# Optimization experiments

Hardware: AMD Instinct MI355X
Metric: run time of the kernel (lower is better)

The kernel has to match this reference:

```python
import jax, jax.numpy as jnp
import numpy as np

B = 16384
C = 512          # mean candidate count per sample
T = B * C        # total flat logits length (static)


def _seg_ce(logits, counts, gt, valid, B):
    """Segmented cross-entropy over variable-length candidate sets.
    logits: [T] flat concatenated logits; counts: [B] segment lengths (sum == T);
    gt: [B] target index within each segment; valid: [B] bool mask.
    Returns (mean loss over valid samples, n_correct, n_valid)."""
    Ttot = logits.shape[0]
    offsets = jnp.cumsum(counts) - counts                       # [B] start of each segment
    seg = jnp.repeat(jnp.arange(B), counts, total_repeat_length=Ttot)  # [T] segment ids
    segmax = jax.ops.segment_max(logits, seg, num_segments=B)   # [B]
    ex = jnp.exp(logits - segmax[seg])
    Z = jax.ops.segment_sum(ex, seg, num_segments=B)            # [B]
    lse = jnp.log(Z) + segmax                                   # [B] logsumexp per segment
    # target logit: clamp position for safety; invalid rows are masked out anyway
    pos = offsets + jnp.clip(gt, 0, jnp.maximum(counts - 1, 0))
    ce = lse - logits[pos]                                      # [B]
    in_range = (gt >= 0) & (gt < counts)
    vmask = (counts > 0) & in_range & valid
    n_valid = vmask.sum()
    loss = jnp.where(vmask, ce, 0.0).sum() / jnp.maximum(n_valid, 1)
    # argmax within each segment (first occurrence, matching torch.argmax)
    local = jnp.arange(Ttot) - offsets[seg]
    is_max = logits == segmax[seg]
    arg = jax.ops.segment_min(jnp.where(is_max, local, Ttot), seg, num_segments=B)
    n_correct = (vmask & (arg == gt)).sum()
    return loss, n_correct, n_valid


def setup_inputs() -> dict:
    key = jax.random.key(0)
    ks = jax.random.split(key, 8)
    # counts alternate C+32 / C-32 so sum == B*C exactly (static T)
    counts = jnp.where(jnp.arange(B) % 2 == 0, C + 32, C - 32).astype(jnp.int32)
    sys_logits = jax.random.normal(ks[0], (T,), dtype=jnp.float32)
    bar_logits = jax.random.normal(ks[1], (T,), dtype=jnp.float32)
    gt_system_idx = jax.random.randint(ks[2], (B,), 0, C - 32).astype(jnp.int32)
    gt_bar_in_sys = jax.random.randint(ks[3], (B,), 0, C - 32).astype(jnp.int32)
    note_positions = jax.random.uniform(ks[4], (B,), dtype=jnp.float32)
    gt_note_position = jax.random.uniform(ks[5], (B,), dtype=jnp.float32)
    gt_valid = jax.random.bernoulli(ks[6], 0.97, (B,))
    return {
        'sys_logits': sys_logits, 'sys_counts': counts,
        'bar_logits': bar_logits, 'bar_counts': counts,
        'note_positions': note_positions,
        'gt_system_idx': gt_system_idx, 'gt_bar_in_sys': gt_bar_in_sys,
        'gt_note_position': gt_note_position, 'gt_valid': gt_valid,
        'log_var_sys': jnp.zeros((), jnp.float32),
        'log_var_bar': jnp.zeros((), jnp.float32),
        'log_var_note': jnp.zeros((), jnp.float32),
    }


def reference(sys_logits, sys_counts, bar_logits, bar_counts, note_positions,
              gt_system_idx, gt_bar_in_sys, gt_note_position, gt_valid,
              log_var_sys, log_var_bar, log_var_note):
    Bn = gt_system_idx.shape[0]
    sys_loss, sys_correct, n_valid = _seg_ce(sys_logits, sys_counts, gt_system_idx, gt_valid, Bn)
    bar_loss, bar_correct, n_valid_bar = _seg_ce(bar_logits, bar_counts, gt_bar_in_sys, gt_valid, Bn)
    # note position MSE over valid samples (bar_valid == gt_valid here)
    m = gt_valid
    nsel = m.sum()
    sq = jnp.where(m, (note_positions - gt_note_position) ** 2, 0.0)
    note_loss = jnp.where(nsel > 0, sq.sum() / jnp.maximum(nsel, 1), 0.0)
    prec_sys = jnp.exp(-log_var_sys)
    prec_bar = jnp.exp(-log_var_bar)
    prec_note = jnp.exp(-log_var_note)
    loss = (0.5 * prec_sys * sys_loss + 0.5 * log_var_sys
            + 0.5 * prec_bar * bar_loss + 0.5 * log_var_bar
            + 0.5 * prec_note * note_loss + 0.5 * log_var_note)
    sys_acc = sys_correct / jnp.maximum(n_valid, 1)
    bar_acc = bar_correct / jnp.maximum(n_valid_bar, 1)
    return (loss, sys_loss, bar_loss, note_loss, sys_acc, bar_acc,
            prec_sys, prec_bar, prec_note)
```

## Files before the change

kernel.cpp:

```cpp
#include <hip/hip_runtime.h>
#include <math.h>

#define SCAN_BLOCKS 64
#define DESC_BASE 512
#define NOTE_SQ   256
#define NOTE_CNT  320

__device__ __forceinline__ bool is_valid(const void* gv, int flag, int i) {
  if (flag == 0) return ((const int*)gv)[i] != 0;
  if (flag == 1) return ((const unsigned char*)gv)[i] != 0;
  return ((const float*)gv)[i] != 0.0f;
}

__global__ __launch_bounds__(256)
void uwl_scan_desc(const int* __restrict__ c_sys, const int* __restrict__ c_bar,
                   const int* __restrict__ gt_sys, const int* __restrict__ gt_bar,
                   const void* __restrict__ gv,
                   const float* __restrict__ npos, const float* __restrict__ gnp,
                   int B, int* __restrict__ wsI, float* __restrict__ wsF) {
  const int blk = blockIdx.x;
  const int lane = threadIdx.x & 63;
  const int wid = threadIdx.x >> 6;
  __shared__ int s_flag;
  __shared__ int baseS, baseB;
  __shared__ int ws1[4], ws2[4];
  __shared__ float fsq[4];
  const int chunk = (B + SCAN_BLOCKS - 1) / SCAN_BLOCKS;
  const int start = blk * chunk;
  const int end = (start + chunk < B) ? start + chunk : B;
  int bs = 0, bb = 0;
  {
    const int s4 = start >> 2;
    const int4* cs4 = (const int4*)c_sys;
    const int4* cb4 = (const int4*)c_bar;
    for (int j = threadIdx.x; j < s4; j += 256) {
      const int4 a = cs4[j]; bs += a.x + a.y + a.z + a.w;
      const int4 b = cb4[j]; bb += b.x + b.y + b.z + b.w;
    }
    if (threadIdx.x < (start & 3)) {
      bs += c_sys[(s4 << 2) + threadIdx.x];
      bb += c_bar[(s4 << 2) + threadIdx.x];
    }
  }
#pragma unroll
  for (int d = 1; d < 64; d <<= 1) {
    bs += __shfl_xor(bs, d, 64);
    bb += __shfl_xor(bb, d, 64);
  }
  if (lane == 0) { ws1[wid] = bs; ws2[wid] = bb; }
  if (threadIdx.x < 64) {
    int nw = B / 4; if (nw > 64) nw = 64; if (nw < 1) nw = 1;
    const unsigned int x =
        (threadIdx.x < nw) ? ((const unsigned int*)gv)[threadIdx.x] : 0u;
    const bool all01 = __all(x <= 1u);
    const bool allf = __all(x == 0u || x == 0x3F800000u);
    if (threadIdx.x == 0) s_flag = all01 ? 0 : (allf ? 2 : 1);
  }
  if (blk == 0) {
    if (threadIdx.x >= 1 && threadIdx.x <= 8) wsI[threadIdx.x * 16] = 0;
    if (threadIdx.x == 9) wsI[144] = 0;
  }
  __syncthreads();
  if (threadIdx.x == 0) {
    baseS = ws1[0] + ws1[1] + ws1[2] + ws1[3];
    baseB = ws2[0] + ws2[1] + ws2[2] + ws2[3];
  }
  __syncthreads();
  const int flag = s_flag;
  int carry1 = baseS, carry2 = baseB;
  int4* descS = (int4*)(wsI + DESC_BASE);
  int4* descB = descS + B;
  for (int base = start; base < end; base += 256) {
    const int idx = base + threadIdx.x;
    const bool ok = idx < end;
    const int x1 = ok ? c_sys[idx] : 0;
    const int x2 = ok ? c_bar[idx] : 0;
    int o1 = x1, o2 = x2;
#pragma unroll
    for (int d = 1; d < 64; d <<= 1) {
      const int v1 = __shfl_up(o1, d, 64);
      const int v2 = __shfl_up(o2, d, 64);
      if (lane >= d) { o1 += v1; o2 += v2; }
    }
    if (lane == 63) { ws1[wid] = o1; ws2[wid] = o2; }
    __syncthreads();
    int w1 = 0, w2 = 0;
    for (int w = 0; w < wid; ++w) { w1 += ws1[w]; w2 += ws2[w]; }
    if (ok) {
      const int g1 = gt_sys[idx], g2 = gt_bar[idx];
      const bool v = is_valid(gv, flag, idx);
      descS[idx] = make_int4(carry1 + w1 + o1 - x1, x1, g1,
                             (x1 > 0 && g1 >= 0 && g1 < x1 && v) ? 1 : 0);
      descB[idx] = make_int4(carry2 + w2 + o2 - x2, x2, g2,
                             (x2 > 0 && g2 >= 0 && g2 < x2 && v) ? 1 : 0);
    }
    carry1 += ws1[0] + ws1[1] + ws1[2] + ws1[3];
    carry2 += ws2[0] + ws2[1] + ws2[2] + ws2[3];
    __syncthreads();
  }
  float sq = 0.f; int cnt = 0;
  for (int i = start + threadIdx.x; i < end; i += 256) {
    if (is_valid(gv, flag, i)) {
      const float d = npos[i] - gnp[i];
      sq += d * d; cnt += 1;
    }
  }
#pragma unroll
  for (int d = 1; d < 64; d <<= 1) {
    sq += __shfl_xor(sq, d, 64);
    cnt += __shfl_xor(cnt, d, 64);
  }
  if (lane == 0) { fsq[wid] = sq; ws1[wid] = cnt; }
  __syncthreads();
  if (threadIdx.x == 0) {
    wsF[NOTE_SQ + blk] = fsq[0] + fsq[1] + fsq[2] + fsq[3];
    wsI[NOTE_CNT + blk] = ws1[0] + ws1[1] + ws1[2] + ws1[3];
  }
}

__global__ __launch_bounds__(256)
void uwl_ce_kernel(const float* __restrict__ sys_lg, const float* __restrict__ bar_lg,
                   int B, int* __restrict__ wsI, float* __restrict__ wsF) {
  const int wave = __builtin_amdgcn_readfirstlane(
      (int)((blockIdx.x * blockDim.x + threadIdx.x) >> 6));
  const int lane = threadIdx.x & 63;
  if (wave >= 2 * B) return;
  const int4 d4 = ((const int4*)(wsI + DESC_BASE))[wave];
  const float* lg = (wave < B) ? sys_lg : bar_lg;
  const int off_i = d4.x, count = d4.y, gt = d4.z, vld = d4.w;
  const long long off = off_i;

  float m = -INFINITY;
  float s = 0.f;
  float tl = 0.f;
  const bool regpath = (count >= 4) && (count <= 576) &&
                       ((off_i & 3) == 0) && ((count & 3) == 0);
  if (regpath) {
    const float4* p = (const float4*)(lg + off);
    const int emax = (count >> 2) - 1;
    float vals[8];
#pragma unroll
    for (int k = 0; k < 2; ++k) {
      const int e4 = (k << 6) + lane;
      const int ec = (e4 > emax) ? emax : e4;
      const float4 v = p[ec];
      const bool live = (e4 <= emax);
      vals[4 * k]     = live ? v.x : -INFINITY;
      vals[4 * k + 1] = live ? v.y : -INFINITY;
      vals[4 * k + 2] = live ? v.z : -INFINITY;
      vals[4 * k + 3] = live ? v.w : -INFINITY;
    }
    const int ti = 512 + lane;
    const int tic = (ti < count) ? ti : (count - 1);
    const float tvr = lg[off + tic];
    const float tv = (ti < count) ? tvr : -INFINITY;
#pragma unroll
    for (int k = 0; k < 8; ++k) m = fmaxf(m, vals[k]);
    m = fmaxf(m, tv);
#pragma unroll
    for (int k = 0; k < 8; ++k) s += __expf(vals[k]);
    s += __expf(tv);
    const int gts = vld ? gt : 0;
    float pick;
    int srclane;
    if (gts < 512) {
      const int q = ((gts >> 8) << 2) | (gts & 3);
      pick = vals[0];
#pragma unroll
      for (int i = 1; i < 8; ++i) pick = (i == q) ? vals[i] : pick;
      srclane = (gts >> 2) & 63;
    } else {
      pick = tv;
      srclane = gts - 512;
    }
    tl = __shfl(pick, srclane, 64);
  } else {
    for (int i = lane; i < count; i += 64) {
      const float v = lg[off + i];
      m = fmaxf(m, v);
      s += __expf(v);
    }
    if (vld) {
      const float t0 = (lane == 0) ? lg[off + gt] : 0.f;
      tl = __shfl(t0, 0, 64);
    }
  }
#pragma unroll
  for (int d = 1; d < 64; d <<= 1) {
    s += __shfl_xor(s, d, 64);
    m = fmaxf(m, __shfl_xor(m, d, 64));
  }
  if (lane == 0) {
    float ce = 0.f, code = 0.f;
    if (vld) {
      ce = __logf(s) - tl;
      code = (tl == m) ? 3.f : 1.f;
    }
    ((float2*)(wsF + DESC_BASE + 8 * B))[wave] = make_float2(ce, code);
  }
}

__global__ __launch_bounds__(256)
void uwl_reduce_kernel(const float* __restrict__ lvs_p, const float* __restrict__ lvb_p,
                       const float* __restrict__ lvn_p,
                       int B, int* wsI, float* wsF, float* __restrict__ out) {
  const float4* pw4 = (const float4*)(wsF + DESC_BASE + 8 * B);
  float ces = 0.f, ceb = 0.f;
  int nvs = 0, cs = 0, nvb = 0, cb = 0;
  const int stride = gridDim.x * blockDim.x;
  for (int j = blockIdx.x * blockDim.x + threadIdx.x; j < B; j += stride) {
    const float4 v = pw4[j];
    const int e0 = 2 * j, e1 = 2 * j + 1;
    const int c0 = (int)v.y, c1 = (int)v.w;
    if (e0 < B) { ces += v.x; nvs += c0 & 1; cs += c0 >> 1; }
    else        { ceb += v.x; nvb += c0 & 1; cb += c0 >> 1; }
    if (e1 < B) { ces += v.z; nvs += c1 & 1; cs += c1 >> 1; }
    else        { ceb += v.z; nvb += c1 & 1; cb += c1 >> 1; }
  }
  float sq = 0.f; int cnt = 0;
  if (blockIdx.x == 0 && threadIdx.x < SCAN_BLOCKS) {
    sq = wsF[NOTE_SQ + threadIdx.x];
    cnt = wsI[NOTE_CNT + threadIdx.x];
  }
#pragma unroll
  for (int d = 1; d < 64; d <<= 1) {
    ces += __shfl_xor(ces, d, 64);
    ceb += __shfl_xor(ceb, d, 64);
    nvs += __shfl_xor(nvs, d, 64);
    cs  += __shfl_xor(cs,  d, 64);
    nvb += __shfl_xor(nvb, d, 64);
    cb  += __shfl_xor(cb,  d, 64);
    sq  += __shfl_xor(sq,  d, 64);
    cnt += __shfl_xor(cnt, d, 64);
  }
  if ((threadIdx.x & 63) == 0) {
    atomicAdd(&wsI[16], nvs);
    atomicAdd(&wsI[32], cs);
    atomicAdd(&wsF[48], ces);
    atomicAdd(&wsI[64], nvb);
    atomicAdd(&wsI[80], cb);
    atomicAdd(&wsF[96], ceb);
    atomicAdd(&wsI[112], cnt);
    atomicAdd(&wsF[128], sq);
  }
  __syncthreads();
  if (threadIdx.x == 0) {
    __threadfence();
    const int t = atomicAdd(&wsI[144], 1);
    if (t == (int)gridDim.x - 1) {
      __threadfence();
      const int fnvs = atomicAdd(&wsI[16], 0);
      const int fcs  = atomicAdd(&wsI[32], 0);
      const int fnvb = atomicAdd(&wsI[64], 0);
      const int fcb  = atomicAdd(&wsI[80], 0);
      const int fnn  = atomicAdd(&wsI[112], 0);
      const float fces = atomicAdd(&wsF[48], 0.f);
      const float fceb = atomicAdd(&wsF[96], 0.f);
      const float fsq  = atomicAdd(&wsF[128], 0.f);
      const float sys_loss = fces / (float)(fnvs > 1 ? fnvs : 1);
      const float bar_loss = fceb / (float)(fnvb > 1 ? fnvb : 1);
      const float note_loss = (fnn > 0) ? fsq / (float)fnn : 0.f;
      const float lvs = lvs_p[0], lvb = lvb_p[0], lvn = lvn_p[0];
      const float ps = expf(-lvs), pb = expf(-lvb), pn = expf(-lvn);
      out[0] = 0.5f * (ps * sys_loss + lvs + pb * bar_loss + lvb + pn * note_loss + lvn);
      out[1] = sys_loss;
      out[2] = bar_loss;
      out[3] = note_loss;
      out[4] = (float)fcs / (float)(fnvs > 1 ? fnvs : 1);
      out[5] = (float)fcb / (float)(fnvb > 1 ? fnvb : 1);
      out[6] = ps;
      out[7] = pb;
      out[8] = pn;
    }
  }
}

extern "C" void kernel_launch(void* const* d_in, const int* in_sizes, int n_in,
                              void* d_out, int out_size, void* d_ws, size_t ws_size,
                              hipStream_t stream) {
  const float* sys_lg = (const float*)d_in[0];
  const int*   c_sys  = (const int*)d_in[1];
  const float* bar_lg = (const float*)d_in[2];
  const int*   c_bar  = (const int*)d_in[3];
  const float* npos   = (const float*)d_in[4];
  const int*   gt_sys = (const int*)d_in[5];
  const int*   gt_bar = (const int*)d_in[6];
  const float* gnp    = (const float*)d_in[7];
  const void*  gv     = d_in[8];
  const float* lvs    = (const float*)d_in[9];
  const float* lvb    = (const float*)d_in[10];
  const float* lvn    = (const float*)d_in[11];
  const int B = in_sizes[1];

  int*   wsI = (int*)d_ws;
  float* wsF = (float*)d_ws;

  uwl_scan_desc<<<SCAN_BLOCKS, 256, 0, stream>>>(c_sys, c_bar, gt_sys, gt_bar, gv,
                                                 npos, gnp, B, wsI, wsF);

  const long long nthreads = (long long)(2 * B) * 64;
  const int nblocks = (int)((nthreads + 255) / 256);
  uwl_ce_kernel<<<nblocks, 256, 0, stream>>>(sys_lg, bar_lg, B, wsI, wsF);

  uwl_reduce_kernel<<<64, 256, 0, stream>>>(lvs, lvb, lvn, B, wsI, wsF, (float*)d_out);
}
```

Before: 130.0 us.

## Widen scan grid, split scan waves by role, make CE kernel grid-stride

The scan/descriptor kernel now runs on 256 blocks instead of 64. Within each block, wave 0 does the segment prefix scan with a single-wave carry and wave 1 computes the note MSE, removing the block-wide barriers inside the scan loop. The CE kernel becomes a persistent grid-stride loop over segments, capped at 2048 blocks, instead of launching one wave per segment. The workspace offsets move to make room for 256 per-block note partials. The trade-offs are two idle waves per scan block and more redundant prefix-count reads across the larger scan grid.

Result: no change. 131.6 us (+1.3%).

```diff
diff --git a/kernel.cpp b/kernel.cpp
--- a/kernel.cpp
+++ b/kernel.cpp
@@ -1,10 +1,10 @@
 #include <hip/hip_runtime.h>
 #include <math.h>
 
-#define SCAN_BLOCKS 64
-#define DESC_BASE 512
+#define SCAN_BLOCKS 256
 #define NOTE_SQ   256
-#define NOTE_CNT  320
+#define NOTE_CNT  512
+#define DESC_BASE 1024
 
 __device__ __forceinline__ bool is_valid(const void* gv, int flag, int i) {
   if (flag == 0) return ((const int*)gv)[i] != 0;
@@ -19,27 +19,38 @@
                    const float* __restrict__ npos, const float* __restrict__ gnp,
                    int B, int* __restrict__ wsI, float* __restrict__ wsF) {
   const int blk = blockIdx.x;
-  const int lane = threadIdx.x & 63;
-  const int wid = threadIdx.x >> 6;
+  const int tid = threadIdx.x;
+  const int lane = tid & 63;
+  const int wid = tid >> 6;
   __shared__ int s_flag;
-  __shared__ int baseS, baseB;
-  __shared__ int ws1[4], ws2[4];
-  __shared__ float fsq[4];
+  __shared__ int sS[4], sB[4];
   const int chunk = (B + SCAN_BLOCKS - 1) / SCAN_BLOCKS;
-  const int start = blk * chunk;
-  const int end = (start + chunk < B) ? start + chunk : B;
+  const int start0 = blk * chunk;
+  const int start = (start0 < B) ? start0 : B;
+  const int end = (start0 + chunk < B) ? start0 + chunk : B;
+  if (tid < 64) {
+    int nw = B / 4; if (nw > 64) nw = 64; if (nw < 1) nw = 1;
+    const unsigned int x = (tid < nw) ? ((const unsigned int*)gv)[tid] : 0u;
+    const bool all01 = __all(x <= 1u);
+    const bool allf = __all(x == 0u || x == 0x3F800000u);
+    if (tid == 0) s_flag = all01 ? 0 : (allf ? 2 : 1);
+  }
+  if (blk == 0) {
+    if (tid >= 1 && tid <= 8) wsI[tid * 16] = 0;
+    if (tid == 9) wsI[144] = 0;
+  }
   int bs = 0, bb = 0;
   {
     const int s4 = start >> 2;
     const int4* cs4 = (const int4*)c_sys;
     const int4* cb4 = (const int4*)c_bar;
-    for (int j = threadIdx.x; j < s4; j += 256) {
+    for (int j = tid; j < s4; j += 256) {
       const int4 a = cs4[j]; bs += a.x + a.y + a.z + a.w;
       const int4 b = cb4[j]; bb += b.x + b.y + b.z + b.w;
     }
-    if (threadIdx.x < (start & 3)) {
-      bs += c_sys[(s4 << 2) + threadIdx.x];
-      bb += c_bar[(s4 << 2) + threadIdx.x];
+    if (tid < (start & 3)) {
+      bs += c_sys[(s4 << 2) + tid];
+      bb += c_bar[(s4 << 2) + tid];
     }
   }
 #pragma unroll
@@ -47,156 +58,138 @@
     bs += __shfl_xor(bs, d, 64);
     bb += __shfl_xor(bb, d, 64);
   }
-  if (lane == 0) { ws1[wid] = bs; ws2[wid] = bb; }
-  if (threadIdx.x < 64) {
-    int nw = B / 4; if (nw > 64) nw = 64; if (nw < 1) nw = 1;
-    const unsigned int x =
-        (threadIdx.x < nw) ? ((const unsigned int*)gv)[threadIdx.x] : 0u;
-    const bool all01 = __all(x <= 1u);
-    const bool allf = __all(x == 0u || x == 0x3F800000u);
-    if (threadIdx.x == 0) s_flag = all01 ? 0 : (allf ? 2 : 1);
-  }
-  if (blk == 0) {
-    if (threadIdx.x >= 1 && threadIdx.x <= 8) wsI[threadIdx.x * 16] = 0;
-    if (threadIdx.x == 9) wsI[144] = 0;
-  }
-  __syncthreads();
-  if (threadIdx.x == 0) {
-    baseS = ws1[0] + ws1[1] + ws1[2] + ws1[3];
-    baseB = ws2[0] + ws2[1] + ws2[2] + ws2[3];
-  }
+  if (lane == 0) { sS[wid] = bs; sB[wid] = bb; }
   __syncthreads();
   const int flag = s_flag;
-  int carry1 = baseS, carry2 = baseB;
-  int4* descS = (int4*)(wsI + DESC_BASE);
-  int4* descB = descS + B;
-  for (int base = start; base < end; base += 256) {
-    const int idx = base + threadIdx.x;
-    const bool ok = idx < end;
-    const int x1 = ok ? c_sys[idx] : 0;
-    const int x2 = ok ? c_bar[idx] : 0;
-    int o1 = x1, o2 = x2;
+  if (wid == 0) {
+    int carry1 = sS[0] + sS[1] + sS[2] + sS[3];
+    int carry2 = sB[0] + sB[1] + sB[2] + sB[3];
+    int4* descS = (int4*)(wsI + DESC_BASE);
+    int4* descB = descS + B;
+    for (int base = start; base < end; base += 64) {
+      const int idx = base + lane;
+      const bool ok = idx < end;
+      const int x1 = ok ? c_sys[idx] : 0;
+      const int x2 = ok ? c_bar[idx] : 0;
+      int o1 = x1, o2 = x2;
+#pragma unroll
+      for (int d = 1; d < 64; d <<= 1) {
+        const int v1 = __shfl_up(o1, d, 64);
+        const int v2 = __shfl_up(o2, d, 64);
+        if (lane >= d) { o1 += v1; o2 += v2; }
+      }
+      if (ok) {
+        const int g1 = gt_sys[idx], g2 = gt_bar[idx];
+        const bool v = is_valid(gv, flag, idx);
+        descS[idx] = make_int4(carry1 + o1 - x1, x1, g1,
+                               (x1 > 0 && g1 >= 0 && g1 < x1 && v) ? 1 : 0);
+        descB[idx] = make_int4(carry2 + o2 - x2, x2, g2,
+                               (x2 > 0 && g2 >= 0 && g2 < x2 && v) ? 1 : 0);
+      }
+      carry1 += __shfl(o1, 63, 64);
+      carry2 += __shfl(o2, 63, 64);
+    }
+  } else if (wid == 1) {
+    float sq = 0.f; int cnt = 0;
+    for (int i = start + lane; i < end; i += 64) {
+      if (is_valid(gv, flag, i)) {
+        const float d = npos[i] - gnp[i];
+        sq += d * d; cnt += 1;
+      }
+    }
 #pragma unroll
     for (int d = 1; d < 64; d <<= 1) {
-      const int v1 = __shfl_up(o1, d, 64);
-      const int v2 = __shfl_up(o2, d, 64);
-      if (lane >= d) { o1 += v1; o2 += v2; }
-    }
-    if (lane == 63) { ws1[wid] = o1; ws2[wid] = o2; }
-    __syncthreads();
-    int w1 = 0, w2 = 0;
-    for (int w = 0; w < wid; ++w) { w1 += ws1[w]; w2 += ws2[w]; }
-    if (ok) {
-      const int g1 = gt_sys[idx], g2 = gt_bar[idx];
-      const bool v = is_valid(gv, flag, idx);
-      descS[idx] = make_int4(carry1 + w1 + o1 - x1, x1, g1,
-                             (x1 > 0 && g1 >= 0 && g1 < x1 && v) ? 1 : 0);
-      descB[idx] = make_int4(carry2 + w2 + o2 - x2, x2, g2,
-                             (x2 > 0 && g2 >= 0 && g2 < x2 && v) ? 1 : 0);
-    }
-    carry1 += ws1[0] + ws1[1] + ws1[2] + ws1[3];
-    carry2 += ws2[0] + ws2[1] + ws2[2] + ws2[3];
-    __syncthreads();
-  }
-  float sq = 0.f; int cnt = 0;
-  for (int i = start + threadIdx.x; i < end; i += 256) {
-    if (is_valid(gv, flag, i)) {
-      const float d = npos[i] - gnp[i];
-      sq += d * d; cnt += 1;
-    }
-  }
-#pragma unroll
-  for (int d = 1; d < 64; d <<= 1) {
-    sq += __shfl_xor(sq, d, 64);
-    cnt += __shfl_xor(cnt, d, 64);
-  }
-  if (lane == 0) { fsq[wid] = sq; ws1[wid] = cnt; }
-  __syncthreads();
-  if (threadIdx.x == 0) {
-    wsF[NOTE_SQ + blk] = fsq[0] + fsq[1] + fsq[2] + fsq[3];
-    wsI[NOTE_CNT + blk] = ws1[0] + ws1[1] + ws1[2] + ws1[3];
+      sq += __shfl_xor(sq, d, 64);
+      cnt += __shfl_xor(cnt, d, 64);
+    }
+    if (lane == 0) {
+      wsF[NOTE_SQ + blk] = sq;
+      wsI[NOTE_CNT + blk] = cnt;
+    }
   }
 }
 
 __global__ __launch_bounds__(256)
 void uwl_ce_kernel(const float* __restrict__ sys_lg, const float* __restrict__ bar_lg,
                    int B, int* __restrict__ wsI, float* __restrict__ wsF) {
-  const int wave = __builtin_amdgcn_readfirstlane(
-      (int)((blockIdx.x * blockDim.x + threadIdx.x) >> 6));
   const int lane = threadIdx.x & 63;
-  if (wave >= 2 * B) return;
-  const int4 d4 = ((const int4*)(wsI + DESC_BASE))[wave];
-  const float* lg = (wave < B) ? sys_lg : bar_lg;
-  const int off_i = d4.x, count = d4.y, gt = d4.z, vld = d4.w;
-  const long long off = off_i;
-
-  float m = -INFINITY;
-  float s = 0.f;
-  float tl = 0.f;
-  const bool regpath = (count >= 4) && (count <= 576) &&
-                       ((off_i & 3) == 0) && ((count & 3) == 0);
-  if (regpath) {
-    const float4* p = (const float4*)(lg + off);
-    const int emax = (count >> 2) - 1;
-    float vals[8];
-#pragma unroll
-    for (int k = 0; k < 2; ++k) {
-      const int e4 = (k << 6) + lane;
-      const int ec = (e4 > emax) ? emax : e4;
-      const float4 v = p[ec];
-      const bool live = (e4 <= emax);
-      vals[4 * k]     = live ? v.x : -INFINITY;
-      vals[4 * k + 1] = live ? v.y : -INFINITY;
-      vals[4 * k + 2] = live ? v.z : -INFINITY;
-      vals[4 * k + 3] = live ? v.w : -INFINITY;
-    }
-    const int ti = 512 + lane;
-    const int tic = (ti < count) ? ti : (count - 1);
-    const float tvr = lg[off + tic];
-    const float tv = (ti < count) ? tvr : -INFINITY;
-#pragma unroll
-    for (int k = 0; k < 8; ++k) m = fmaxf(m, vals[k]);
-    m = fmaxf(m, tv);
-#pragma unroll
-    for (int k = 0; k < 8; ++k) s += __expf(vals[k]);
-    s += __expf(tv);
-    const int gts = vld ? gt : 0;
-    float pick;
-    int srclane;
-    if (gts < 512) {
-      const int q = ((gts >> 8) << 2) | (gts & 3);
-      pick = vals[0];
-#pragma unroll
-      for (int i = 1; i < 8; ++i) pick = (i == q) ? vals[i] : pick;
-      srclane = (gts >> 2) & 63;
+  const int wid = threadIdx.x >> 6;
+  const int wstep = (int)(gridDim.x << 2);
+  for (int wave0 = (int)(blockIdx.x << 2) + wid; wave0 < 2 * B; wave0 += wstep) {
+    const int wave = __builtin_amdgcn_readfirstlane(wave0);
+    const int4 d4 = ((const int4*)(wsI + DESC_BASE))[wave];
+    const float* lg = (wave < B) ? sys_lg : bar_lg;
+    const int off_i = d4.x, count = d4.y, gt = d4.z, vld = d4.w;
+    const long long off = off_i;
+
+    float m = -INFINITY;
+    float s = 0.f;
+    float tl = 0.f;
+    const bool regpath = (count >= 4) && (count <= 576) &&
+                         ((off_i & 3) == 0) && ((count & 3) == 0);
+    if (regpath) {
+      const float4* p = (const float4*)(lg + off);
+      const int emax = (count >> 2) - 1;
+      float vals[8];
+#pragma unroll
+      for (int k = 0; k < 2; ++k) {
+        const int e4 = (k << 6) + lane;
+        const int ec = (e4 > emax) ? emax : e4;
+        const float4 v = p[ec];
+        const bool live = (e4 <= emax);
+        vals[4 * k]     = live ? v.x : -INFINITY;
+        vals[4 * k + 1] = live ? v.y : -INFINITY;
+        vals[4 * k + 2] = live ? v.z : -INFINITY;
+        vals[4 * k + 3] = live ? v.w : -INFINITY;
+      }
+      const int ti = 512 + lane;
+      const int tic = (ti < count) ? ti : (count - 1);
+      const float tvr = lg[off + tic];
+      const float tv = (ti < count) ? tvr : -INFINITY;
+#pragma unroll
+      for (int k = 0; k < 8; ++k) m = fmaxf(m, vals[k]);
+      m = fmaxf(m, tv);
+#pragma unroll
+      for (int k = 0; k < 8; ++k) s += __expf(vals[k]);
+      s += __expf(tv);
+      const int gts = vld ? gt : 0;
+      float pick;
+      int srclane;
+      if (gts < 512) {
+        const int q = ((gts >> 8) << 2) | (gts & 3);
+        pick = vals[0];
+#pragma unroll
+        for (int i = 1; i < 8; ++i) pick = (i == q) ? vals[i] : pick;
+        srclane = (gts >> 2) & 63;
+      } else {
+        pick = tv;
+        srclane = gts - 512;
+      }
+      tl = __shfl(pick, srclane, 64);
     } else {
-      pick = tv;
-      srclane = gts - 512;
-    }
-    tl = __shfl(pick, srclane, 64);
-  } else {
-    for (int i = lane; i < count; i += 64) {
-      const float v = lg[off + i];
-      m = fmaxf(m, v);
-      s += __expf(v);
-    }
-    if (vld) {
-      const float t0 = (lane == 0) ? lg[off + gt] : 0.f;
-      tl = __shfl(t0, 0, 64);
-    }
-  }
-#pragma unroll
-  for (int d = 1; d < 64; d <<= 1) {
-    s += __shfl_xor(s, d, 64);
-    m = fmaxf(m, __shfl_xor(m, d, 64));
-  }
-  if (lane == 0) {
-    float ce = 0.f, code = 0.f;
-    if (vld) {
-      ce = __logf(s) - tl;
-      code = (tl == m) ? 3.f : 1.f;
-    }
-    ((float2*)(wsF + DESC_BASE + 8 * B))[wave] = make_float2(ce, code);
+      for (int i = lane; i < count; i += 64) {
+        const float v = lg[off + i];
+        m = fmaxf(m, v);
+        s += __expf(v);
+      }
+      if (vld) {
+        const float t0 = (lane == 0) ? lg[off + gt] : 0.f;
+        tl = __shfl(t0, 0, 64);
+      }
+    }
+#pragma unroll
+    for (int d = 1; d < 64; d <<= 1) {
+      s += __shfl_xor(s, d, 64);
+      m = fmaxf(m, __shfl_xor(m, d, 64));
+    }
+    if (lane == 0) {
+      float ce = 0.f, code = 0.f;
+      if (vld) {
+        ce = __logf(s) - tl;
+        code = (tl == m) ? 3.f : 1.f;
+      }
+      ((float2*)(wsF + DESC_BASE + 8 * B))[wave] = make_float2(ce, code);
+    }
   }
 }
 
@@ -298,8 +291,9 @@
   uwl_scan_desc<<<SCAN_BLOCKS, 256, 0, stream>>>(c_sys, c_bar, gt_sys, gt_bar, gv,
                                                  npos, gnp, B, wsI, wsF);
 
-  const long long nthreads = (long long)(2 * B) * 64;
-  const int nblocks = (int)((nthreads + 255) / 256);
+  const long long nwaveslots = ((long long)(2 * B) + 3) / 4;
+  int nblocks = (int)((nwaveslots < 2048) ? nwaveslots : 2048);
+  if (nblocks < 1) nblocks = 1;
   uwl_ce_kernel<<<nblocks, 256, 0, stream>>>(sys_lg, bar_lg, B, wsI, wsF);
 
   uwl_reduce_kernel<<<64, 256, 0, stream>>>(lvs, lvb, lvn, B, wsI, wsF, (float*)d_out);
```
